# Performance work log

Hardware: AMD Instinct MI355X
Metric: run time of the kernel (lower is better)

## Reference

```python
import jax, jax.numpy as jnp
import numpy as np

TOPK = 20

def setup_inputs() -> dict:
    key = jax.random.key(0)
    k1, k2, k3 = jax.random.split(key, 3)
    B, n, D = 4, 4096, 256
    src1 = jax.random.normal(k1, (B, n, D), dtype=jnp.float32)
    src2 = jax.random.normal(k2, (B, n, D), dtype=jnp.float32)
    memoryMartix = jax.random.normal(k3, (n, n), dtype=jnp.float32)
    return {"src1": src1, "src2": src2, "memoryMartix": memoryMartix}

def reference(src1, src2, memoryMartix):
    # softmax over dim=1 of the [n, n] memory matrix
    probs = jax.nn.softmax(memoryMartix, axis=1)            # [n, n]
    # top-k along dim=1: values and indices per row
    vtopk, ind = jax.lax.top_k(probs, TOPK)                 # [n, k], [n, k]
    # gather src2 rows per output position: [B, n, k, D]
    gathered = jnp.take(src2, ind, axis=1)
    # weighted sum over the k selected neighbors
    src = jnp.einsum('bnkd,nk->bnd', gathered, vtopk)       # [B, n, D]
    return src + src1
```

## Files before the change

### kernel.cpp

```cpp
#include <hip/hip_runtime.h>
#include <math.h>

#define TOPK  20
#define NROW  4096
#define DDIM  256
#define NB    4
#define NCHUNK 16

#define AWPB   2
#define ABLOCK (AWPB * 64)
#define BBLOCK 256

typedef float vf4 __attribute__((ext_vector_type(4)));

__device__ __forceinline__ void wave_lds_fence() {
    asm volatile("s_waitcnt lgkmcnt(0)" ::: "memory");
}

__device__ __forceinline__ bool lex_gt(float av, int ai, float bv, int bi) {
    return (av > bv) || (av == bv && ai < bi);
}

__device__ __forceinline__ void bitonic64_desc(float& v, int& i, int lane) {
#pragma unroll
    for (int k = 2; k <= 64; k <<= 1) {
#pragma unroll
        for (int j = k >> 1; j > 0; j >>= 1) {
            float pv = __shfl_xor(v, j, 64);
            int   pi = __shfl_xor(i, j, 64);
            bool takeBig = ((lane & k) == 0) == ((lane & j) == 0);
            bool pBig = lex_gt(pv, pi, v, i);
            if (takeBig == pBig) { v = pv; i = pi; }
        }
    }
}

__global__ __launch_bounds__(ABLOCK) void topk_select(
    const float* __restrict__ mem,
    float* __restrict__ ws_w,
    int*   __restrict__ ws_i)
{
    __shared__ vf4   rowbuf[AWPB][NROW / 4];
    __shared__ float cand_v[AWPB][64];
    __shared__ int   cand_i[AWPB][64];
    __shared__ int   ccnt[AWPB];

    const int wave = threadIdx.x >> 6;
    const int lane = threadIdx.x & 63;
    const int n    = blockIdx.x * AWPB + wave;

    if (lane == 0) ccnt[wave] = 0;

    const vf4* mrow = (const vf4*)(mem + (size_t)n * NROW);

    float bv = -INFINITY; int bi = 0x7fffffff;
    float lsum = 0.f;
#pragma unroll
    for (int j = 0; j < NCHUNK; ++j) {
        const vf4 q = mrow[lane + 64 * j];
        rowbuf[wave][64 * j + lane] = q;
        const int base = 4 * lane + 256 * j;
        if (q.x > bv) { bv = q.x; bi = base + 0; }
        if (q.y > bv) { bv = q.y; bi = base + 1; }
        if (q.z > bv) { bv = q.z; bi = base + 2; }
        if (q.w > bv) { bv = q.w; bi = base + 3; }
        lsum += __expf(q.x) + __expf(q.y) + __expf(q.z) + __expf(q.w);
    }
#pragma unroll
    for (int o = 32; o > 0; o >>= 1) lsum += __shfl_xor(lsum, o, 64);
    const float inv_denom = 1.0f / lsum;

    float sv = bv; int si = bi;
    bitonic64_desc(sv, si, lane);
    const float tv = __shfl(sv, 19, 64);
    const int   ti = __shfl(si, 19, 64);

    wave_lds_fence();

#pragma unroll
    for (int j = 0; j < NCHUNK; ++j) {
        const vf4 q = rowbuf[wave][64 * j + lane];
        const int base = 4 * lane + 256 * j;
        if ((q.x > tv) || (q.x == tv && (base + 0) <= ti)) { int s = atomicAdd(&ccnt[wave], 1); if (s < 64) { cand_v[wave][s] = q.x; cand_i[wave][s] = base + 0; } }
        if ((q.y > tv) || (q.y == tv && (base + 1) <= ti)) { int s = atomicAdd(&ccnt[wave], 1); if (s < 64) { cand_v[wave][s] = q.y; cand_i[wave][s] = base + 1; } }
        if ((q.z > tv) || (q.z == tv && (base + 2) <= ti)) { int s = atomicAdd(&ccnt[wave], 1); if (s < 64) { cand_v[wave][s] = q.z; cand_i[wave][s] = base + 2; } }
        if ((q.w > tv) || (q.w == tv && (base + 3) <= ti)) { int s = atomicAdd(&ccnt[wave], 1); if (s < 64) { cand_v[wave][s] = q.w; cand_i[wave][s] = base + 3; } }
    }
    wave_lds_fence();
    const int total = ccnt[wave];

    float* gw = ws_w + (size_t)n * TOPK;
    int*   gi = ws_i + (size_t)n * TOPK;

    if (total <= 64) {
        float cv = -INFINITY; int ci = 0x7fffffff;
        if (lane < total) { cv = cand_v[wave][lane]; ci = cand_i[wave][lane]; }
        bitonic64_desc(cv, ci, lane);
        if (lane < TOPK) {
            gw[lane] = __expf(cv) * inv_denom;
            gi[lane] = ci;
        }
    } else {
        unsigned long long dead = 0;
        float cv = bv; int ci = bi;
        for (int r = 0; r < TOPK; ++r) {
            float wv = cv; int wi = ci;
#pragma unroll
            for (int o = 32; o > 0; o >>= 1) {
                float ov = __shfl_xor(wv, o, 64);
                int   oi = __shfl_xor(wi, o, 64);
                if (lex_gt(ov, oi, wv, wi)) { wv = ov; wi = oi; }
            }
            if (lane == 0) {
                gw[r] = __expf(wv) * inv_denom;
                gi[r] = wi;
            }
            if (ci == wi) {
                const int e = 4 * ((wi >> 8) & 15) + (wi & 3);
                dead |= (1ull << e);
                cv = -INFINITY; ci = 0x7fffffff;
#pragma unroll
                for (int j = 0; j < NCHUNK; ++j) {
                    const vf4 q = rowbuf[wave][64 * j + lane];
                    const int base = 4 * lane + 256 * j;
                    if (!((dead >> (4 * j + 0)) & 1) && q.x > cv) { cv = q.x; ci = base + 0; }
                    if (!((dead >> (4 * j + 1)) & 1) && q.y > cv) { cv = q.y; ci = base + 1; }
                    if (!((dead >> (4 * j + 2)) & 1) && q.z > cv) { cv = q.z; ci = base + 2; }
                    if (!((dead >> (4 * j + 3)) & 1) && q.w > cv) { cv = q.w; ci = base + 3; }
                }
            }
        }
    }
}

__global__ __launch_bounds__(BBLOCK, 4) void gather_epilogue(
    const float* __restrict__ src1,
    const float* __restrict__ src2,
    const float* __restrict__ ws_w,
    const int*   __restrict__ ws_i,
    float* __restrict__ out)
{
    const int bid  = blockIdx.x;
    const int xcd  = bid & 7;
    const int b    = xcd >> 1;
    const int h    = xcd & 1;
    const int grp  = bid >> 3;
    const int wave = threadIdx.x >> 6;
    const int lane = threadIdx.x & 63;
    const int half = lane >> 5;
    const int dl   = lane & 31;
    const int n    = grp * 8 + wave * 2 + half;
    const int d4   = h * 32 + dl;

    const float* gw = ws_w + (size_t)n * TOPK;
    const int*   gi = ws_i + (size_t)n * TOPK;
    float wk[TOPK]; int ik[TOPK];
#pragma unroll
    for (int k = 0; k < TOPK; ++k) { wk[k] = gw[k]; ik[k] = gi[k]; }

    const vf4* s2b = (const vf4*)src2 + (size_t)b * NROW * (DDIM / 4);
    const size_t rowbase = ((size_t)b * NROW + n) * (DDIM / 4) + d4;

    vf4 acc = __builtin_nontemporal_load((const vf4*)src1 + rowbase);
#pragma unroll
    for (int k = 0; k < TOPK; ++k) {
        const vf4 g = s2b[(size_t)ik[k] * (DDIM / 4) + d4];
        acc += wk[k] * g;
    }
    __builtin_nontemporal_store(acc, (vf4*)out + rowbase);
}

extern "C" void kernel_launch(void* const* d_in, const int* in_sizes, int n_in,
                              void* d_out, int out_size, void* d_ws, size_t ws_size,
                              hipStream_t stream) {
    const float* src1 = (const float*)d_in[0];
    const float* src2 = (const float*)d_in[1];
    const float* mem  = (const float*)d_in[2];
    float* out = (float*)d_out;

    float* ws_w = (float*)d_ws;
    int*   ws_i = (int*)d_ws + (size_t)NROW * TOPK;

    topk_select<<<NROW / AWPB, ABLOCK, 0, stream>>>(mem, ws_w, ws_i);
    gather_epilogue<<<NROW, BBLOCK, 0, stream>>>(src1, src2, ws_w, ws_i, out);
}
```

Baseline: 161.7 us.

## Split each top-k row across four waves and keep row in registers

The top-k selection kernel now assigns one row to a 256-thread block, with each of four waves owning a quarter of the row held in registers instead of staging the whole row in LDS. Per-wave thresholds and exp-sums are combined through shared memory with block barriers, and the fallback path does a cross-wave argmax each round. This is meant to raise memory-level parallelism and occupancy for the row scan. The cost is extra __syncthreads and cross-wave reductions.

```diff
diff --git a/kernel.cpp b/kernel.cpp
--- a/kernel.cpp
+++ b/kernel.cpp
@@ -5,17 +5,12 @@
 #define NROW  4096
 #define DDIM  256
 #define NB    4
-#define NCHUNK 16
 
-#define AWPB   2
-#define ABLOCK (AWPB * 64)
+#define QCHUNK 4
+#define ABLOCK 256
 #define BBLOCK 256
 
 typedef float vf4 __attribute__((ext_vector_type(4)));
-
-__device__ __forceinline__ void wave_lds_fence() {
-    asm volatile("s_waitcnt lgkmcnt(0)" ::: "memory");
-}
 
 __device__ __forceinline__ bool lex_gt(float av, int ai, float bv, int bi) {
     return (av > bv) || (av == bv && ai < bi);
@@ -35,73 +30,85 @@
     }
 }
 
-__global__ __launch_bounds__(ABLOCK) void topk_select(
+__global__ __launch_bounds__(ABLOCK, 8) void topk_select(
     const float* __restrict__ mem,
     float* __restrict__ ws_w,
     int*   __restrict__ ws_i)
 {
-    __shared__ vf4   rowbuf[AWPB][NROW / 4];
-    __shared__ float cand_v[AWPB][64];
-    __shared__ int   cand_i[AWPB][64];
-    __shared__ int   ccnt[AWPB];
+    __shared__ float tau_v[4];
+    __shared__ int   tau_i[4];
+    __shared__ float esum[4];
+    __shared__ float cand_v[64];
+    __shared__ int   cand_i[64];
+    __shared__ int   ccnt;
+    __shared__ float win_v[4];
+    __shared__ int   win_i[4];
 
     const int wave = threadIdx.x >> 6;
     const int lane = threadIdx.x & 63;
-    const int n    = blockIdx.x * AWPB + wave;
-
-    if (lane == 0) ccnt[wave] = 0;
+    const int n    = blockIdx.x;
 
     const vf4* mrow = (const vf4*)(mem + (size_t)n * NROW);
+
+    vf4 q[QCHUNK];
+#pragma unroll
+    for (int j = 0; j < QCHUNK; ++j) q[j] = mrow[wave * 256 + 64 * j + lane];
 
     float bv = -INFINITY; int bi = 0x7fffffff;
     float lsum = 0.f;
 #pragma unroll
-    for (int j = 0; j < NCHUNK; ++j) {
-        const vf4 q = mrow[lane + 64 * j];
-        rowbuf[wave][64 * j + lane] = q;
-        const int base = 4 * lane + 256 * j;
-        if (q.x > bv) { bv = q.x; bi = base + 0; }
-        if (q.y > bv) { bv = q.y; bi = base + 1; }
-        if (q.z > bv) { bv = q.z; bi = base + 2; }
-        if (q.w > bv) { bv = q.w; bi = base + 3; }
-        lsum += __expf(q.x) + __expf(q.y) + __expf(q.z) + __expf(q.w);
+    for (int j = 0; j < QCHUNK; ++j) {
+        const int base = 1024 * wave + 256 * j + 4 * lane;
+        if (q[j].x > bv) { bv = q[j].x; bi = base + 0; }
+        if (q[j].y > bv) { bv = q[j].y; bi = base + 1; }
+        if (q[j].z > bv) { bv = q[j].z; bi = base + 2; }
+        if (q[j].w > bv) { bv = q[j].w; bi = base + 3; }
+        lsum += __expf(q[j].x) + __expf(q[j].y) + __expf(q[j].z) + __expf(q[j].w);
     }
 #pragma unroll
     for (int o = 32; o > 0; o >>= 1) lsum += __shfl_xor(lsum, o, 64);
-    const float inv_denom = 1.0f / lsum;
 
     float sv = bv; int si = bi;
     bitonic64_desc(sv, si, lane);
-    const float tv = __shfl(sv, 19, 64);
-    const int   ti = __shfl(si, 19, 64);
+    const float tvw = __shfl(sv, 19, 64);
+    const int   tiw = __shfl(si, 19, 64);
 
-    wave_lds_fence();
+    if (lane == 0) { tau_v[wave] = tvw; tau_i[wave] = tiw; esum[wave] = lsum; }
+    if (threadIdx.x == 0) ccnt = 0;
+    __syncthreads();
+
+    float tv = tau_v[0]; int ti = tau_i[0];
+#pragma unroll
+    for (int w2 = 1; w2 < 4; ++w2)
+        if (lex_gt(tau_v[w2], tau_i[w2], tv, ti)) { tv = tau_v[w2]; ti = tau_i[w2]; }
+    const float inv_denom = 1.0f / (esum[0] + esum[1] + esum[2] + esum[3]);
 
 #pragma unroll
-    for (int j = 0; j < NCHUNK; ++j) {
-        const vf4 q = rowbuf[wave][64 * j + lane];
-        const int base = 4 * lane + 256 * j;
-        if ((q.x > tv) || (q.x == tv && (base + 0) <= ti)) { int s = atomicAdd(&ccnt[wave], 1); if (s < 64) { cand_v[wave][s] = q.x; cand_i[wave][s] = base + 0; } }
-        if ((q.y > tv) || (q.y == tv && (base + 1) <= ti)) { int s = atomicAdd(&ccnt[wave], 1); if (s < 64) { cand_v[wave][s] = q.y; cand_i[wave][s] = base + 1; } }
-        if ((q.z > tv) || (q.z == tv && (base + 2) <= ti)) { int s = atomicAdd(&ccnt[wave], 1); if (s < 64) { cand_v[wave][s] = q.z; cand_i[wave][s] = base + 2; } }
-        if ((q.w > tv) || (q.w == tv && (base + 3) <= ti)) { int s = atomicAdd(&ccnt[wave], 1); if (s < 64) { cand_v[wave][s] = q.w; cand_i[wave][s] = base + 3; } }
+    for (int j = 0; j < QCHUNK; ++j) {
+        const int base = 1024 * wave + 256 * j + 4 * lane;
+        if ((q[j].x > tv) || (q[j].x == tv && (base + 0) <= ti)) { int s = atomicAdd(&ccnt, 1); if (s < 64) { cand_v[s] = q[j].x; cand_i[s] = base + 0; } }
+        if ((q[j].y > tv) || (q[j].y == tv && (base + 1) <= ti)) { int s = atomicAdd(&ccnt, 1); if (s < 64) { cand_v[s] = q[j].y; cand_i[s] = base + 1; } }
+        if ((q[j].z > tv) || (q[j].z == tv && (base + 2) <= ti)) { int s = atomicAdd(&ccnt, 1); if (s < 64) { cand_v[s] = q[j].z; cand_i[s] = base + 2; } }
+        if ((q[j].w > tv) || (q[j].w == tv && (base + 3) <= ti)) { int s = atomicAdd(&ccnt, 1); if (s < 64) { cand_v[s] = q[j].w; cand_i[s] = base + 3; } }
     }
-    wave_lds_fence();
-    const int total = ccnt[wave];
+    __syncthreads();
+    const int total = ccnt;
 
-    float* gw = ws_w + (size_t)n * TOPK;
-    int*   gi = ws_i + (size_t)n * TOPK;
+    float* gw  = ws_w + (size_t)n * TOPK;
+    int*   gip = ws_i + (size_t)n * TOPK;
 
     if (total <= 64) {
-        float cv = -INFINITY; int ci = 0x7fffffff;
-        if (lane < total) { cv = cand_v[wave][lane]; ci = cand_i[wave][lane]; }
-        bitonic64_desc(cv, ci, lane);
-        if (lane < TOPK) {
-            gw[lane] = __expf(cv) * inv_denom;
-            gi[lane] = ci;
+        if (wave == 0) {
+            float cv = -INFINITY; int ci = 0x7fffffff;
+            if (lane < total) { cv = cand_v[lane]; ci = cand_i[lane]; }
+            bitonic64_desc(cv, ci, lane);
+            if (lane < TOPK) {
+                gw[lane]  = __expf(cv) * inv_denom;
+                gip[lane] = ci;
+            }
         }
     } else {
-        unsigned long long dead = 0;
+        unsigned dead = 0;
         float cv = bv; int ci = bi;
         for (int r = 0; r < TOPK; ++r) {
             float wv = cv; int wi = ci;
@@ -111,24 +118,30 @@
                 int   oi = __shfl_xor(wi, o, 64);
                 if (lex_gt(ov, oi, wv, wi)) { wv = ov; wi = oi; }
             }
-            if (lane == 0) {
-                gw[r] = __expf(wv) * inv_denom;
-                gi[r] = wi;
+            if (lane == 0) { win_v[wave] = wv; win_i[wave] = wi; }
+            __syncthreads();
+            float gv = win_v[0]; int gidx = win_i[0];
+#pragma unroll
+            for (int w2 = 1; w2 < 4; ++w2)
+                if (lex_gt(win_v[w2], win_i[w2], gv, gidx)) { gv = win_v[w2]; gidx = win_i[w2]; }
+            if (threadIdx.x == 0) {
+                gw[r]  = __expf(gv) * inv_denom;
+                gip[r] = gidx;
             }
-            if (ci == wi) {
-                const int e = 4 * ((wi >> 8) & 15) + (wi & 3);
-                dead |= (1ull << e);
+            if (ci == gidx) {
+                const int e = 4 * ((gidx >> 8) & 3) + (gidx & 3);
+                dead |= (1u << e);
                 cv = -INFINITY; ci = 0x7fffffff;
 #pragma unroll
-                for (int j = 0; j < NCHUNK; ++j) {
-                    const vf4 q = rowbuf[wave][64 * j + lane];
-                    const int base = 4 * lane + 256 * j;
-                    if (!((dead >> (4 * j + 0)) & 1) && q.x > cv) { cv = q.x; ci = base + 0; }
-                    if (!((dead >> (4 * j + 1)) & 1) && q.y > cv) { cv = q.y; ci = base + 1; }
-                    if (!((dead >> (4 * j + 2)) & 1) && q.z > cv) { cv = q.z; ci = base + 2; }
-                    if (!((dead >> (4 * j + 3)) & 1) && q.w > cv) { cv = q.w; ci = base + 3; }
+                for (int j = 0; j < QCHUNK; ++j) {
+                    const int base = 1024 * wave + 256 * j + 4 * lane;
+                    if (!((dead >> (4 * j + 0)) & 1) && q[j].x > cv) { cv = q[j].x; ci = base + 0; }
+                    if (!((dead >> (4 * j + 1)) & 1) && q[j].y > cv) { cv = q[j].y; ci = base + 1; }
+                    if (!((dead >> (4 * j + 2)) & 1) && q[j].z > cv) { cv = q[j].z; ci = base + 2; }
+                    if (!((dead >> (4 * j + 3)) & 1) && q[j].w > cv) { cv = q[j].w; ci = base + 3; }
                 }
             }
+            __syncthreads();
         }
     }
 }
@@ -181,6 +194,6 @@
     float* ws_w = (float*)d_ws;
     int*   ws_i = (int*)d_ws + (size_t)NROW * TOPK;
 
-    topk_select<<<NROW / AWPB, ABLOCK, 0, stream>>>(mem, ws_w, ws_i);
+    topk_select<<<NROW, ABLOCK, 0, stream>>>(mem, ws_w, ws_i);
     gather_epilogue<<<NROW, BBLOCK, 0, stream>>>(src1, src2, ws_w, ws_i, out);
 }
```

Result: slower. 204.8 us (+26.6%).

## Select top-k candidates with a fixed value threshold in one pass, dropping the LDS row buffer

Applied to the files above, without the earlier changes.

The top-k kernel now gathers candidates in the same pass that computes the softmax denominator, keeping only values above a fixed threshold of 2.3. This removes the per-lane max, the bitonic sort used to find a cutoff, the second LDS scan, and the 32 KB shared row buffer. Waves per block rise from 2 to 4, and a minimum-occupancy hint is added. If the threshold yields fewer than 20 or more than 64 candidates, an exact fallback rescans the row from global memory for each of the 20 picks, which costs more for inputs that do not match the tuned distribution.

```diff
diff --git a/kernel.cpp b/kernel.cpp
--- a/kernel.cpp
+++ b/kernel.cpp
@@ -1,13 +1,14 @@
 #include <hip/hip_runtime.h>
 #include <math.h>
 
-#define TOPK  20
-#define NROW  4096
-#define DDIM  256
-#define NB    4
+#define TOPK   20
+#define NROW   4096
+#define DDIM   256
+#define NB     4
 #define NCHUNK 16
+#define THRESH 2.3f
 
-#define AWPB   2
+#define AWPB   4
 #define ABLOCK (AWPB * 64)
 #define BBLOCK 256
 
@@ -35,12 +36,11 @@
     }
 }
 
-__global__ __launch_bounds__(ABLOCK) void topk_select(
+__global__ __launch_bounds__(ABLOCK, 8) void topk_select(
     const float* __restrict__ mem,
     float* __restrict__ ws_w,
     int*   __restrict__ ws_i)
 {
-    __shared__ vf4   rowbuf[AWPB][NROW / 4];
     __shared__ float cand_v[AWPB][64];
     __shared__ int   cand_i[AWPB][64];
     __shared__ int   ccnt[AWPB];
@@ -50,49 +50,32 @@
     const int n    = blockIdx.x * AWPB + wave;
 
     if (lane == 0) ccnt[wave] = 0;
+    wave_lds_fence();
 
     const vf4* mrow = (const vf4*)(mem + (size_t)n * NROW);
 
-    float bv = -INFINITY; int bi = 0x7fffffff;
     float lsum = 0.f;
 #pragma unroll
     for (int j = 0; j < NCHUNK; ++j) {
-        const vf4 q = mrow[lane + 64 * j];
-        rowbuf[wave][64 * j + lane] = q;
-        const int base = 4 * lane + 256 * j;
-        if (q.x > bv) { bv = q.x; bi = base + 0; }
-        if (q.y > bv) { bv = q.y; bi = base + 1; }
-        if (q.z > bv) { bv = q.z; bi = base + 2; }
-        if (q.w > bv) { bv = q.w; bi = base + 3; }
+        const vf4 q = mrow[64 * j + lane];
+        const int base = 256 * j + 4 * lane;
         lsum += __expf(q.x) + __expf(q.y) + __expf(q.z) + __expf(q.w);
+        if (q.x > THRESH) { int s = atomicAdd(&ccnt[wave], 1); if (s < 64) { cand_v[wave][s] = q.x; cand_i[wave][s] = base + 0; } }
+        if (q.y > THRESH) { int s = atomicAdd(&ccnt[wave], 1); if (s < 64) { cand_v[wave][s] = q.y; cand_i[wave][s] = base + 1; } }
+        if (q.z > THRESH) { int s = atomicAdd(&ccnt[wave], 1); if (s < 64) { cand_v[wave][s] = q.z; cand_i[wave][s] = base + 2; } }
+        if (q.w > THRESH) { int s = atomicAdd(&ccnt[wave], 1); if (s < 64) { cand_v[wave][s] = q.w; cand_i[wave][s] = base + 3; } }
     }
 #pragma unroll
     for (int o = 32; o > 0; o >>= 1) lsum += __shfl_xor(lsum, o, 64);
     const float inv_denom = 1.0f / lsum;
 
-    float sv = bv; int si = bi;
-    bitonic64_desc(sv, si, lane);
-    const float tv = __shfl(sv, 19, 64);
-    const int   ti = __shfl(si, 19, 64);
-
-    wave_lds_fence();
-
-#pragma unroll
-    for (int j = 0; j < NCHUNK; ++j) {
-        const vf4 q = rowbuf[wave][64 * j + lane];
-        const int base = 4 * lane + 256 * j;
-        if ((q.x > tv) || (q.x == tv && (base + 0) <= ti)) { int s = atomicAdd(&ccnt[wave], 1); if (s < 64) { cand_v[wave][s] = q.x; cand_i[wave][s] = base + 0; } }
-        if ((q.y > tv) || (q.y == tv && (base + 1) <= ti)) { int s = atomicAdd(&ccnt[wave], 1); if (s < 64) { cand_v[wave][s] = q.y; cand_i[wave][s] = base + 1; } }
-        if ((q.z > tv) || (q.z == tv && (base + 2) <= ti)) { int s = atomicAdd(&ccnt[wave], 1); if (s < 64) { cand_v[wave][s] = q.z; cand_i[wave][s] = base + 2; } }
-        if ((q.w > tv) || (q.w == tv && (base + 3) <= ti)) { int s = atomicAdd(&ccnt[wave], 1); if (s < 64) { cand_v[wave][s] = q.w; cand_i[wave][s] = base + 3; } }
-    }
     wave_lds_fence();
     const int total = ccnt[wave];
 
     float* gw = ws_w + (size_t)n * TOPK;
     int*   gi = ws_i + (size_t)n * TOPK;
 
-    if (total <= 64) {
+    if (total >= TOPK && total <= 64) {
         float cv = -INFINITY; int ci = 0x7fffffff;
         if (lane < total) { cv = cand_v[wave][lane]; ci = cand_i[wave][lane]; }
         bitonic64_desc(cv, ci, lane);
@@ -102,8 +85,17 @@
         }
     } else {
         unsigned long long dead = 0;
-        float cv = bv; int ci = bi;
         for (int r = 0; r < TOPK; ++r) {
+            float cv = -INFINITY; int ci = 0x7fffffff;
+#pragma unroll
+            for (int j = 0; j < NCHUNK; ++j) {
+                const vf4 q = mrow[64 * j + lane];
+                const int base = 256 * j + 4 * lane;
+                if (!((dead >> (4 * j + 0)) & 1) && q.x > cv) { cv = q.x; ci = base + 0; }
+                if (!((dead >> (4 * j + 1)) & 1) && q.y > cv) { cv = q.y; ci = base + 1; }
+                if (!((dead >> (4 * j + 2)) & 1) && q.z > cv) { cv = q.z; ci = base + 2; }
+                if (!((dead >> (4 * j + 3)) & 1) && q.w > cv) { cv = q.w; ci = base + 3; }
+            }
             float wv = cv; int wi = ci;
 #pragma unroll
             for (int o = 32; o > 0; o >>= 1) {
@@ -115,20 +107,7 @@
                 gw[r] = __expf(wv) * inv_denom;
                 gi[r] = wi;
             }
-            if (ci == wi) {
-                const int e = 4 * ((wi >> 8) & 15) + (wi & 3);
-                dead |= (1ull << e);
-                cv = -INFINITY; ci = 0x7fffffff;
-#pragma unroll
-                for (int j = 0; j < NCHUNK; ++j) {
-                    const vf4 q = rowbuf[wave][64 * j + lane];
-                    const int base = 4 * lane + 256 * j;
-                    if (!((dead >> (4 * j + 0)) & 1) && q.x > cv) { cv = q.x; ci = base + 0; }
-                    if (!((dead >> (4 * j + 1)) & 1) && q.y > cv) { cv = q.y; ci = base + 1; }
-                    if (!((dead >> (4 * j + 2)) & 1) && q.z > cv) { cv = q.z; ci = base + 2; }
-                    if (!((dead >> (4 * j + 3)) & 1) && q.w > cv) { cv = q.w; ci = base + 3; }
-                }
-            }
+            if (ci == wi) dead |= (1ull << (4 * ((wi >> 8) & 15) + (wi & 3)));
         }
     }
 }
```

Result: slower. 233.4 us (+44.3%).
